# Kernel optimization log

Hardware: AMD Instinct MI355X
Metric: run time of the kernel (lower is better)

The kernel has to match this reference:

```python
import jax, jax.numpy as jnp
import numpy as np

B, S, D_IN, D = 4, 4096, 512, 256


def setup_inputs() -> dict:
    key = jax.random.key(0)
    ks = jax.random.split(key, 7)
    return {
        "query": jax.random.normal(ks[0], (B, S, D_IN), dtype=jnp.float32),
        "key": jax.random.normal(ks[1], (B, S, D_IN), dtype=jnp.float32),
        "value": jax.random.normal(ks[2], (B, S, D), dtype=jnp.float32),
        "Wq": jax.random.normal(ks[3], (D, D_IN), dtype=jnp.float32) * (1.0 / np.sqrt(D_IN)),
        "bq": jax.random.normal(ks[4], (D,), dtype=jnp.float32) * 0.01,
        "Wk": jax.random.normal(ks[5], (D, D_IN), dtype=jnp.float32) * (1.0 / np.sqrt(D_IN)),
        "bk": jax.random.normal(ks[6], (D,), dtype=jnp.float32) * 0.01,
        "scale_factor": jnp.ones((), dtype=jnp.float32),  # source uses scale_factor = 1
        "dropout_p": 0,  # fixed to 0 -> dropout is identity (deterministic baseline)
    }


def reference(query, key, value, Wq, bq, Wk, bk, scale_factor, dropout_p):
    # q/k linear projections: [B,S,512] -> [B,S,256]
    q = jnp.einsum("bsi,di->bsd", query, Wq) + bq
    k = jnp.einsum("bsi,di->bsd", key, Wk) + bk
    # scaled dot-product attention scores [B,S,S]
    scores = jnp.einsum("bqd,bkd->bqk", q, k) * scale_factor
    attn = jax.nn.softmax(scores, axis=-1)
    # dropout_p == 0 -> identity
    out = jnp.einsum("bqk,bkd->bqd", attn, value)
    return out
```

## Files before the change

### kernel.cpp

```cpp
#include <hip/hip_runtime.h>

#define S_LEN 4096
#define NROWS 16384

typedef float f32x4 __attribute__((ext_vector_type(4)));
typedef _Float16 f16x8 __attribute__((ext_vector_type(8)));

__device__ __forceinline__ unsigned short f2h(float f) {
  _Float16 h = (_Float16)f;
  return __builtin_bit_cast(unsigned short, h);
}

__device__ __forceinline__ void gload16(const void* g, void* l) {
  __builtin_amdgcn_global_load_lds(
      (const __attribute__((address_space(1))) void*)g,
      (__attribute__((address_space(3))) void*)l, 16, 0, 0);
}

__global__ void cw_kernel(const float* __restrict__ Wq, const float* __restrict__ Wk,
                          unsigned short* __restrict__ Wqb, unsigned short* __restrict__ Wkb) {
  const int i = (blockIdx.x * 256 + threadIdx.x) * 8;
  if (i >= 131072) return;
  unsigned short tmp[8] __attribute__((aligned(16)));
#pragma unroll
  for (int u = 0; u < 8; ++u) tmp[u] = f2h(Wq[i + u]);
  *(uint4*)(Wqb + i) = ((const uint4*)tmp)[0];
#pragma unroll
  for (int u = 0; u < 8; ++u) tmp[u] = f2h(Wk[i + u]);
  *(uint4*)(Wkb + i) = ((const uint4*)tmp)[0];
}

__global__ __launch_bounds__(256) void vt_kernel(const float* __restrict__ V,
                                                 unsigned short* __restrict__ Vt) {
  __shared__ float tile[64][65];
  const int tid = threadIdx.x;
  const int b = blockIdx.z, s0 = blockIdx.x * 64, d0 = blockIdx.y * 64;
  {
    const int r = tid >> 2, cs = (tid & 3) * 16;
    const float* src = V + ((long)b * S_LEN + s0 + r) * 256 + d0 + cs;
#pragma unroll
    for (int u = 0; u < 4; ++u) {
      const f32x4 v = __builtin_nontemporal_load((const f32x4*)(src + 4 * u));
      tile[r][cs + 4 * u + 0] = v[0]; tile[r][cs + 4 * u + 1] = v[1];
      tile[r][cs + 4 * u + 2] = v[2]; tile[r][cs + 4 * u + 3] = v[3];
    }
  }
  __syncthreads();
  {
    const int d = tid >> 2, ss = (tid & 3) * 16;
    unsigned short tmp[16] __attribute__((aligned(16)));
#pragma unroll
    for (int u = 0; u < 16; ++u) tmp[u] = f2h(tile[ss + u][d]);
    unsigned short* dst = Vt + ((long)b * 256 + d0 + d) * S_LEN + s0 + ss;
    *(uint4*)dst = ((const uint4*)tmp)[0];
    *((uint4*)dst + 1) = ((const uint4*)tmp)[1];
  }
}

__global__ __launch_bounds__(256, 4) void proj_kernel(
    const float* __restrict__ Xq, const float* __restrict__ Xk,
    const unsigned short* __restrict__ Wqb, const unsigned short* __restrict__ Wkb,
    const float* __restrict__ bq, const float* __restrict__ bk,
    unsigned short* __restrict__ Qb, unsigned short* __restrict__ Kb,
    const float* __restrict__ scale_ptr) {
  const int tid = threadIdx.x;
  const int lane = tid & 63, w = tid >> 6;
  const int h = lane >> 4, cc = lane & 15;
  const int z = blockIdx.y;
  const float* X = z ? Xk : Xq;
  const unsigned short* Wb = z ? Wkb : Wqb;
  const float* bias = z ? bk : bq;
  unsigned short* out = z ? Kb : Qb;
  const float sc = z ? 1.f : scale_ptr[0];
  const int rowbase = blockIdx.x * 64;

  __shared__ char sx[8192];
  __shared__ char sw[32768];

  f32x4 acc[16];
  const f32x4 fz = {0.f, 0.f, 0.f, 0.f};
#pragma unroll
  for (int nf = 0; nf < 16; ++nf) acc[nf] = fz;

  for (int kstep = 0; kstep < 8; ++kstep) {
    const int k0 = kstep * 64;
    __syncthreads();
    {
      const int r = tid >> 2;
      const int cb0 = (tid & 3) * 2;
      const float* src = X + (long)(rowbase + r) * 512 + k0 + (tid & 3) * 16;
      float xv[16];
#pragma unroll
      for (int u = 0; u < 4; ++u) {
        const f32x4 v = __builtin_nontemporal_load((const f32x4*)(src + 4 * u));
        xv[4 * u + 0] = v[0]; xv[4 * u + 1] = v[1];
        xv[4 * u + 2] = v[2]; xv[4 * u + 3] = v[3];
      }
      unsigned short tmp[16] __attribute__((aligned(16)));
#pragma unroll
      for (int u = 0; u < 16; ++u) tmp[u] = f2h(xv[u]);
      *(uint4*)(sx + r * 128 + ((cb0 ^ (r & 7)) * 16)) = ((const uint4*)tmp)[0];
      *(uint4*)(sx + r * 128 + (((cb0 + 1) ^ (r & 7)) * 16)) = ((const uint4*)tmp)[1];
    }
#pragma unroll
    for (int i = 0; i < 8; ++i) {
      const int off = w * 8192 + i * 1024 + lane * 16;
      const int row = off >> 7;
      const int lcb = (lane & 7) ^ (row & 7);
      gload16(Wb + (long)row * 512 + k0 + lcb * 8, sw + w * 8192 + i * 1024);
    }
    __syncthreads();
#pragma unroll
    for (int ks = 0; ks < 2; ++ks) {
      const int rl = 16 * w + cc;
      const f16x8 af = *(const f16x8*)(sx + rl * 128 + (((h + 4 * ks) ^ (rl & 7)) * 16));
#pragma unroll
      for (int nf = 0; nf < 16; ++nf) {
        const int n = cc + 16 * nf;
        const f16x8 bf = *(const f16x8*)(sw + n * 128 + (((h + 4 * ks) ^ (n & 7)) * 16));
        acc[nf] = __builtin_amdgcn_mfma_f32_16x16x32_f16(af, bf, acc[nf], 0, 0, 0);
      }
    }
  }
#pragma unroll
  for (int nf = 0; nf < 16; ++nf) {
    const float bv = bias[cc + 16 * nf];
#pragma unroll
    for (int r = 0; r < 4; ++r) {
      const long grow = rowbase + 16 * w + 4 * h + r;
      out[grow * 256 + cc + 16 * nf] = f2h((acc[nf][r] + bv) * sc);
    }
  }
}

__global__ __launch_bounds__(256, 2) void attn_kernel(
    const unsigned short* __restrict__ Qb, const unsigned short* __restrict__ Kb,
    const unsigned short* __restrict__ Vt, float* __restrict__ out0,
    float* __restrict__ partials, float2* __restrict__ stats,
    int* __restrict__ cnt, int nsplit, int nchunks) {
  extern __shared__ char smem[];
  const int tid = threadIdx.x;
  const int lane = tid & 63, w = tid >> 6;
  const int h = lane >> 4, c = lane & 15;

  int* s_item_p = (int*)(smem + 69632);
  if (tid == 0) {
    const unsigned x = __builtin_amdgcn_s_getreg(6164) & 7u;
    const int pref = (int)x * nchunks / 8;
    int item = 0;
    for (int k = 0; k < nchunks; ++k) {
      const int ch = (pref + k) % nchunks;
      const int t = atomicAdd(cnt + ch, 1);
      if (t < 32) { item = ch * 32 + t; break; }
    }
    *s_item_p = item;
  }
  __syncthreads();
  const int nid = *s_item_p;
  const int gqt = nid & 255;
  const int split = nid >> 8;

  const int b = gqt >> 6;
  const int qrow0 = (gqt & 63) * 64;
  const long brow = (long)b * S_LEN;

  const int kv_len = S_LEN / nsplit;
  const int kv0 = split * kv_len;
  const int nit = kv_len / 32;

  f16x8 qf[8];
  {
    const unsigned short* qbase = Qb + (brow + qrow0 + w * 16 + c) * 256 + h * 8;
#pragma unroll
    for (int kk = 0; kk < 8; ++kk)
      qf[kk] = *(const f16x8*)(qbase + kk * 32);
  }

  f32x4 O[16];
  float mrun[4], lrun[4];
  const f32x4 fz = {0.f, 0.f, 0.f, 0.f};
#pragma unroll
  for (int nfd = 0; nfd < 16; ++nfd) O[nfd] = fz;
#pragma unroll
  for (int r = 0; r < 4; ++r) { mrun[r] = -1e30f; lrun[r] = 0.f; }

  const unsigned short* kbB = Kb + brow * 256;
  const unsigned short* vbB = Vt + (long)b * 256 * S_LEN;

  auto stage = [&](int buf, int it) {
    const int kvb = kv0 + it * 32;
#pragma unroll
    for (int i = 0; i < 4; ++i) {
      const int off = i * 4096 + tid * 16;
      {
        const int row = off >> 9;
        const int lcb = ((off >> 4) & 31) ^ (row & 7);
        gload16(kbB + (long)(kvb + row) * 256 + lcb * 8, smem + buf * 16384 + off);
      }
      {
        const int drow = off >> 6;
        const int lcb = ((off >> 4) & 3) ^ ((drow >> 1) & 3);
        gload16(vbB + (long)drow * S_LEN + kvb + lcb * 8,
                smem + 32768 + buf * 16384 + off);
      }
    }
  };

  char* const pt = smem + 65536 + w * 1024;

  stage(0, 0);
  __syncthreads();

  for (int t = 0; t < nit; ++t) {
    const int buf = t & 1;
    if (t + 1 < nit) stage(buf ^ 1, t + 1);
    const char* kt = smem + buf * 16384;
    const char* vl = smem + 32768 + buf * 16384;

    f32x4 s[2];
    s[0] = fz; s[1] = fz;
    __builtin_amdgcn_s_setprio(1);
#pragma unroll
    for (int kk = 0; kk < 8; ++kk) {
#pragma unroll
      for (int nf = 0; nf < 2; ++nf) {
        const int r = c + 16 * nf;
        const int cb = ((4 * kk + h) ^ (r & 7)) & 31;
        const f16x8 kf = *(const f16x8*)(kt + r * 512 + cb * 16);
        s[nf] = __builtin_amdgcn_mfma_f32_16x16x32_f16(qf[kk], kf, s[nf], 0, 0, 0);
      }
    }
    __builtin_amdgcn_s_setprio(0);

    {
      bool ok = true;
#pragma unroll
      for (int r = 0; r < 4; ++r)
        ok &= (fmaxf(s[0][r], s[1][r]) <= mrun[r] + 8.f);
      if (__all(ok)) {
#pragma unroll
        for (int r = 0; r < 4; ++r) {
          const float p0 = __expf(s[0][r] - mrun[r]);
          const float p1 = __expf(s[1][r] - mrun[r]);
          s[0][r] = p0; s[1][r] = p1;
          lrun[r] += p0 + p1;
        }
      } else {
#pragma unroll
        for (int r = 0; r < 4; ++r) {
          float mx = fmaxf(s[0][r], s[1][r]);
          mx = fmaxf(mx, __shfl_xor(mx, 1));
          mx = fmaxf(mx, __shfl_xor(mx, 2));
          mx = fmaxf(mx, __shfl_xor(mx, 4));
          mx = fmaxf(mx, __shfl_xor(mx, 8));
          const float mnew = fmaxf(mrun[r], mx);
          const float alpha = __expf(mrun[r] - mnew);
          const float p0 = __expf(s[0][r] - mnew);
          const float p1 = __expf(s[1][r] - mnew);
          s[0][r] = p0; s[1][r] = p1;
          lrun[r] = lrun[r] * alpha + p0 + p1;
          mrun[r] = mnew;
#pragma unroll
          for (int nfd = 0; nfd < 16; ++nfd) O[nfd][r] *= alpha;
        }
      }
#pragma unroll
      for (int nf = 0; nf < 2; ++nf)
#pragma unroll
        for (int r = 0; r < 4; ++r) {
          const int C = c + 16 * nf;
          const int blk = ((C >> 3) ^ r ^ h) & 3;
          *(unsigned short*)(pt + (4 * h + r) * 64 + blk * 16 + (C & 7) * 2) =
              f2h(s[nf][r]);
        }
    }
    asm volatile("" ::: "memory");

    __builtin_amdgcn_s_setprio(1);
    {
      const f16x8 pa = *(const f16x8*)(pt + c * 64 + (((h ^ c ^ (c >> 2)) & 3) * 16));
#pragma unroll
      for (int nfd = 0; nfd < 16; ++nfd) {
        const int dr = c + 16 * nfd;
        const f16x8 vf = *(const f16x8*)(vl + dr * 64 + (((h ^ (dr >> 1)) & 3) * 16));
        O[nfd] = __builtin_amdgcn_mfma_f32_16x16x32_f16(pa, vf, O[nfd], 0, 0, 0);
      }
    }
    __builtin_amdgcn_s_setprio(0);
    __syncthreads();
  }

#pragma unroll
  for (int r = 0; r < 4; ++r) {
    float l = lrun[r];
    l += __shfl_xor(l, 1); l += __shfl_xor(l, 2);
    l += __shfl_xor(l, 4); l += __shfl_xor(l, 8);
    lrun[r] = l;
  }

  const long rowg0 = brow + qrow0 + w * 16 + 4 * h;
  if (nsplit == 1) {
    float inv[4];
#pragma unroll
    for (int r = 0; r < 4; ++r) inv[r] = 1.f / lrun[r];
#pragma unroll
    for (int nfd = 0; nfd < 16; ++nfd)
#pragma unroll
      for (int r = 0; r < 4; ++r)
        out0[(rowg0 + r) * 256 + c + 16 * nfd] = O[nfd][r] * inv[r];
  } else {
    float* dst = (split == 0) ? out0 : (partials + (long)(split - 1) * NROWS * 256);
#pragma unroll
    for (int nfd = 0; nfd < 16; ++nfd)
#pragma unroll
      for (int r = 0; r < 4; ++r)
        dst[(rowg0 + r) * 256 + c + 16 * nfd] = O[nfd][r];
    if (c == 0) {
#pragma unroll
      for (int r = 0; r < 4; ++r)
        stats[(long)split * NROWS + rowg0 + r] = make_float2(mrun[r], lrun[r]);
    }
  }
}

__global__ __launch_bounds__(256) void merge_kernel(float* __restrict__ out0,
                                                    const float* __restrict__ partials,
                                                    const float2* __restrict__ stats,
                                                    int nsplit) {
  const int i4 = blockIdx.x * 256 + threadIdx.x;
  const int row = i4 >> 6;
  float2 st[4];
#pragma unroll
  for (int s = 0; s < 4; ++s)
    st[s] = (s < nsplit) ? stats[s * NROWS + row] : make_float2(-1e30f, 0.f);
  const float m = fmaxf(fmaxf(st[0].x, st[1].x), fmaxf(st[2].x, st[3].x));
  float e[4], den = 0.f;
#pragma unroll
  for (int s = 0; s < 4; ++s) { e[s] = __expf(st[s].x - m); den += st[s].y * e[s]; }
  const float invd = 1.f / den;
  float ax = 0.f, ay = 0.f, az = 0.f, aw = 0.f;
#pragma unroll
  for (int s = 0; s < 4; ++s) {
    if (s < nsplit) {
      const float* src = (s == 0) ? (const float*)out0
                                  : partials + (long)(s - 1) * NROWS * 256;
      const f32x4 v = ((const f32x4*)src)[i4];
      ax += v[0] * e[s]; ay += v[1] * e[s]; az += v[2] * e[s]; aw += v[3] * e[s];
    }
  }
  const f32x4 res = {ax * invd, ay * invd, az * invd, aw * invd};
  ((f32x4*)out0)[i4] = res;
}

extern "C" void kernel_launch(void* const* d_in, const int* in_sizes, int n_in,
                              void* d_out, int out_size, void* d_ws, size_t ws_size,
                              hipStream_t stream) {
  const float* query = (const float*)d_in[0];
  const float* key   = (const float*)d_in[1];
  const float* value = (const float*)d_in[2];
  const float* Wq    = (const float*)d_in[3];
  const float* bq    = (const float*)d_in[4];
  const float* Wk    = (const float*)d_in[5];
  const float* bk    = (const float*)d_in[6];
  const float* scale = (const float*)d_in[7];
  float* out = (float*)d_out;

  char* ws = (char*)d_ws;
  unsigned short* Wqb = (unsigned short*)(ws);
  unsigned short* Wkb = (unsigned short*)(ws + 262144);
  unsigned short* Qb  = (unsigned short*)(ws + 524288);
  unsigned short* Kb  = (unsigned short*)(ws + 8912896);
  unsigned short* Vt  = (unsigned short*)(ws + 17301504);
  int* cnt            = (int*)(ws + 25690112);
  float2* stats       = (float2*)(ws + 25694208);
  float* partials     = (float*)(ws + 26218496);

  int nsplit = 1;
  if (ws_size >= 42995712) nsplit = 2;
  const int nblk = 256 * nsplit;
  const int nchunks = nblk / 32;

  hipMemsetAsync(cnt, 0, 64, stream);
  cw_kernel<<<64, 256, 0, stream>>>(Wq, Wk, Wqb, Wkb);
  vt_kernel<<<dim3(64, 4, 4), 256, 0, stream>>>(value, Vt);
  proj_kernel<<<dim3(256, 2), 256, 0, stream>>>(query, key, Wqb, Wkb, bq, bk, Qb, Kb, scale);

  hipFuncSetAttribute((const void*)attn_kernel,
                      hipFuncAttributeMaxDynamicSharedMemorySize, 69648);
  attn_kernel<<<nblk, 256, 69648, stream>>>(Qb, Kb, Vt, out, partials,
                                            stats, cnt, nsplit, nchunks);
  if (nsplit > 1)
    merge_kernel<<<4096, 256, 0, stream>>>(out, partials, stats, nsplit);
}
```

Before: 186.3 us.

## Split attention warps into 2x2 query/KV tiles with shared softmax and exp2

The attention kernel now arranges its four waves as pairs. Each pair handles 32 query rows, and within a pair each wave takes half of the 32-key tile and half of the output D columns. K fragments are loaded once and reused across two query m-tiles, and V fragments are reused the same way, which cuts LDS reads per MFMA. The cost is extra block barriers each iteration: one for a block-wide fast-path vote, one for exchanging row maxima, and one for the shared P tile. The query scale is also premultiplied by log2(e) so exp2f can replace __expf, and merge is updated to match.

```diff
diff --git a/kernel.cpp b/kernel.cpp
--- a/kernel.cpp
+++ b/kernel.cpp
@@ -71,7 +71,7 @@
   const unsigned short* Wb = z ? Wkb : Wqb;
   const float* bias = z ? bk : bq;
   unsigned short* out = z ? Kb : Qb;
-  const float sc = z ? 1.f : scale_ptr[0];
+  const float sc = z ? 1.f : scale_ptr[0] * 1.44269504088896340736f;
   const int rowbase = blockIdx.x * 64;
 
   __shared__ char sx[8192];
@@ -142,8 +142,9 @@
   const int tid = threadIdx.x;
   const int lane = tid & 63, w = tid >> 6;
   const int h = lane >> 4, c = lane & 15;
-
-  int* s_item_p = (int*)(smem + 69632);
+  const int p = w >> 1, kvh = w & 1;
+
+  int* s_item_p = (int*)(smem + 71184);
   if (tid == 0) {
     const unsigned x = __builtin_amdgcn_s_getreg(6164) & 7u;
     const int pref = (int)x * nchunks / 8;
@@ -168,21 +169,26 @@
   const int kv0 = split * kv_len;
   const int nit = kv_len / 32;
 
-  f16x8 qf[8];
+  f16x8 qf[2][8];
   {
-    const unsigned short* qbase = Qb + (brow + qrow0 + w * 16 + c) * 256 + h * 8;
-#pragma unroll
-    for (int kk = 0; kk < 8; ++kk)
-      qf[kk] = *(const f16x8*)(qbase + kk * 32);
-  }
-
-  f32x4 O[16];
-  float mrun[4], lrun[4];
+    const unsigned short* qbase = Qb + (brow + qrow0 + p * 32 + c) * 256 + h * 8;
+#pragma unroll
+    for (int m = 0; m < 2; ++m)
+#pragma unroll
+      for (int kk = 0; kk < 8; ++kk)
+        qf[m][kk] = *(const f16x8*)(qbase + m * 4096 + kk * 32);
+  }
+
+  f32x4 O[2][8];
+  float mrun[2][4], lrun[2][4];
   const f32x4 fz = {0.f, 0.f, 0.f, 0.f};
 #pragma unroll
-  for (int nfd = 0; nfd < 16; ++nfd) O[nfd] = fz;
-#pragma unroll
-  for (int r = 0; r < 4; ++r) { mrun[r] = -1e30f; lrun[r] = 0.f; }
+  for (int m = 0; m < 2; ++m) {
+#pragma unroll
+    for (int nfd = 0; nfd < 8; ++nfd) O[m][nfd] = fz;
+#pragma unroll
+    for (int r = 0; r < 4; ++r) { mrun[m][r] = -1e30f; lrun[m][r] = 0.f; }
+  }
 
   const unsigned short* kbB = Kb + brow * 256;
   const unsigned short* vbB = Vt + (long)b * 256 * S_LEN;
@@ -206,7 +212,9 @@
     }
   };
 
-  char* const pt = smem + 65536 + w * 1024;
+  char* const ppt = smem + 65536 + p * 2560;
+  float* const comm = (float*)(smem + 70656 + p * 256);
+  int* const okb = (int*)(smem + 71168);
 
   stage(0, 0);
   __syncthreads();
@@ -222,68 +230,91 @@
     __builtin_amdgcn_s_setprio(1);
 #pragma unroll
     for (int kk = 0; kk < 8; ++kk) {
-#pragma unroll
-      for (int nf = 0; nf < 2; ++nf) {
-        const int r = c + 16 * nf;
-        const int cb = ((4 * kk + h) ^ (r & 7)) & 31;
-        const f16x8 kf = *(const f16x8*)(kt + r * 512 + cb * 16);
-        s[nf] = __builtin_amdgcn_mfma_f32_16x16x32_f16(qf[kk], kf, s[nf], 0, 0, 0);
-      }
+      const int krow = kvh * 16 + c;
+      const int cb = ((4 * kk + h) ^ (c & 7)) & 31;
+      const f16x8 kf = *(const f16x8*)(kt + krow * 512 + cb * 16);
+      s[0] = __builtin_amdgcn_mfma_f32_16x16x32_f16(qf[0][kk], kf, s[0], 0, 0, 0);
+      s[1] = __builtin_amdgcn_mfma_f32_16x16x32_f16(qf[1][kk], kf, s[1], 0, 0, 0);
     }
     __builtin_amdgcn_s_setprio(0);
 
-    {
-      bool ok = true;
-#pragma unroll
-      for (int r = 0; r < 4; ++r)
-        ok &= (fmaxf(s[0][r], s[1][r]) <= mrun[r] + 8.f);
-      if (__all(ok)) {
+    bool ok = true;
+#pragma unroll
+    for (int m = 0; m < 2; ++m)
+#pragma unroll
+      for (int r = 0; r < 4; ++r) ok &= (s[m][r] <= mrun[m][r] + 8.f);
+    const int okw = __all(ok) ? 1 : 0;
+    if (lane == 0) okb[w] = okw;
+    asm volatile("s_waitcnt lgkmcnt(0)" ::: "memory");
+    __builtin_amdgcn_sched_barrier(0);
+    __builtin_amdgcn_s_barrier();
+    const int blockfast = okb[0] & okb[1] & okb[2] & okb[3];
+
+    if (blockfast) {
+#pragma unroll
+      for (int m = 0; m < 2; ++m)
 #pragma unroll
         for (int r = 0; r < 4; ++r) {
-          const float p0 = __expf(s[0][r] - mrun[r]);
-          const float p1 = __expf(s[1][r] - mrun[r]);
-          s[0][r] = p0; s[1][r] = p1;
-          lrun[r] += p0 + p1;
+          const float pp = exp2f(s[m][r] - mrun[m][r]);
+          lrun[m][r] += pp;
+          *(unsigned short*)(ppt + (16 * m + 4 * h + r) * 80 + kvh * 32 + c * 2) =
+              f2h(pp);
         }
-      } else {
+    } else {
+      float lm[2][4];
+#pragma unroll
+      for (int m = 0; m < 2; ++m)
 #pragma unroll
         for (int r = 0; r < 4; ++r) {
-          float mx = fmaxf(s[0][r], s[1][r]);
+          float mx = s[m][r];
           mx = fmaxf(mx, __shfl_xor(mx, 1));
           mx = fmaxf(mx, __shfl_xor(mx, 2));
           mx = fmaxf(mx, __shfl_xor(mx, 4));
           mx = fmaxf(mx, __shfl_xor(mx, 8));
-          const float mnew = fmaxf(mrun[r], mx);
-          const float alpha = __expf(mrun[r] - mnew);
-          const float p0 = __expf(s[0][r] - mnew);
-          const float p1 = __expf(s[1][r] - mnew);
-          s[0][r] = p0; s[1][r] = p1;
-          lrun[r] = lrun[r] * alpha + p0 + p1;
-          mrun[r] = mnew;
-#pragma unroll
-          for (int nfd = 0; nfd < 16; ++nfd) O[nfd][r] *= alpha;
+          lm[m][r] = mx;
         }
-      }
-#pragma unroll
-      for (int nf = 0; nf < 2; ++nf)
+      if (c == 0) {
+#pragma unroll
+        for (int m = 0; m < 2; ++m)
+#pragma unroll
+          for (int r = 0; r < 4; ++r)
+            comm[kvh * 32 + 16 * m + 4 * h + r] = lm[m][r];
+      }
+      asm volatile("s_waitcnt lgkmcnt(0)" ::: "memory");
+      __builtin_amdgcn_sched_barrier(0);
+      __builtin_amdgcn_s_barrier();
+#pragma unroll
+      for (int m = 0; m < 2; ++m)
 #pragma unroll
         for (int r = 0; r < 4; ++r) {
-          const int C = c + 16 * nf;
-          const int blk = ((C >> 3) ^ r ^ h) & 3;
-          *(unsigned short*)(pt + (4 * h + r) * 64 + blk * 16 + (C & 7) * 2) =
-              f2h(s[nf][r]);
+          const float pmx = comm[(kvh ^ 1) * 32 + 16 * m + 4 * h + r];
+          const float mnew = fmaxf(mrun[m][r], fmaxf(lm[m][r], pmx));
+          const float alpha = exp2f(mrun[m][r] - mnew);
+          const float pp = exp2f(s[m][r] - mnew);
+          lrun[m][r] = lrun[m][r] * alpha + pp;
+          mrun[m][r] = mnew;
+#pragma unroll
+          for (int nfd = 0; nfd < 8; ++nfd) O[m][nfd][r] *= alpha;
+          *(unsigned short*)(ppt + (16 * m + 4 * h + r) * 80 + kvh * 32 + c * 2) =
+              f2h(pp);
         }
     }
-    asm volatile("" ::: "memory");
+    asm volatile("s_waitcnt lgkmcnt(0)" ::: "memory");
+    __builtin_amdgcn_sched_barrier(0);
+    __builtin_amdgcn_s_barrier();
 
     __builtin_amdgcn_s_setprio(1);
     {
-      const f16x8 pa = *(const f16x8*)(pt + c * 64 + (((h ^ c ^ (c >> 2)) & 3) * 16));
-#pragma unroll
-      for (int nfd = 0; nfd < 16; ++nfd) {
-        const int dr = c + 16 * nfd;
+      f16x8 pa[2];
+#pragma unroll
+      for (int m = 0; m < 2; ++m)
+        pa[m] = *(const f16x8*)(ppt + (16 * m + c) * 80 + h * 16);
+#pragma unroll
+      for (int nfd = 0; nfd < 8; ++nfd) {
+        const int dr = kvh * 128 + c + 16 * nfd;
         const f16x8 vf = *(const f16x8*)(vl + dr * 64 + (((h ^ (dr >> 1)) & 3) * 16));
-        O[nfd] = __builtin_amdgcn_mfma_f32_16x16x32_f16(pa, vf, O[nfd], 0, 0, 0);
+        O[0][nfd] = __builtin_amdgcn_mfma_f32_16x16x32_f16(pa[0], vf, O[0][nfd], 0, 0, 0);
+        O[1][nfd] = __builtin_amdgcn_mfma_f32_16x16x32_f16(pa[1], vf, O[1][nfd], 0, 0, 0);
       }
     }
     __builtin_amdgcn_s_setprio(0);
@@ -291,34 +322,59 @@
   }
 
 #pragma unroll
-  for (int r = 0; r < 4; ++r) {
-    float l = lrun[r];
-    l += __shfl_xor(l, 1); l += __shfl_xor(l, 2);
-    l += __shfl_xor(l, 4); l += __shfl_xor(l, 8);
-    lrun[r] = l;
-  }
-
-  const long rowg0 = brow + qrow0 + w * 16 + 4 * h;
+  for (int m = 0; m < 2; ++m)
+#pragma unroll
+    for (int r = 0; r < 4; ++r) {
+      float l = lrun[m][r];
+      l += __shfl_xor(l, 1); l += __shfl_xor(l, 2);
+      l += __shfl_xor(l, 4); l += __shfl_xor(l, 8);
+      lrun[m][r] = l;
+    }
+  if (c == 0) {
+#pragma unroll
+    for (int m = 0; m < 2; ++m)
+#pragma unroll
+      for (int r = 0; r < 4; ++r)
+        comm[kvh * 32 + 16 * m + 4 * h + r] = lrun[m][r];
+  }
+  __syncthreads();
+  float lt[2][4];
+#pragma unroll
+  for (int m = 0; m < 2; ++m)
+#pragma unroll
+    for (int r = 0; r < 4; ++r)
+      lt[m][r] = lrun[m][r] + comm[(kvh ^ 1) * 32 + 16 * m + 4 * h + r];
+
+  const long rowg0 = brow + qrow0 + p * 32 + 4 * h;
   if (nsplit == 1) {
-    float inv[4];
-#pragma unroll
-    for (int r = 0; r < 4; ++r) inv[r] = 1.f / lrun[r];
-#pragma unroll
-    for (int nfd = 0; nfd < 16; ++nfd)
-#pragma unroll
-      for (int r = 0; r < 4; ++r)
-        out0[(rowg0 + r) * 256 + c + 16 * nfd] = O[nfd][r] * inv[r];
+#pragma unroll
+    for (int m = 0; m < 2; ++m) {
+      float inv[4];
+#pragma unroll
+      for (int r = 0; r < 4; ++r) inv[r] = 1.f / lt[m][r];
+#pragma unroll
+      for (int nfd = 0; nfd < 8; ++nfd)
+#pragma unroll
+        for (int r = 0; r < 4; ++r)
+          out0[(rowg0 + 16 * m + r) * 256 + kvh * 128 + c + 16 * nfd] =
+              O[m][nfd][r] * inv[r];
+    }
   } else {
     float* dst = (split == 0) ? out0 : (partials + (long)(split - 1) * NROWS * 256);
 #pragma unroll
-    for (int nfd = 0; nfd < 16; ++nfd)
-#pragma unroll
-      for (int r = 0; r < 4; ++r)
-        dst[(rowg0 + r) * 256 + c + 16 * nfd] = O[nfd][r];
-    if (c == 0) {
-#pragma unroll
-      for (int r = 0; r < 4; ++r)
-        stats[(long)split * NROWS + rowg0 + r] = make_float2(mrun[r], lrun[r]);
+    for (int m = 0; m < 2; ++m)
+#pragma unroll
+      for (int nfd = 0; nfd < 8; ++nfd)
+#pragma unroll
+        for (int r = 0; r < 4; ++r)
+          dst[(rowg0 + 16 * m + r) * 256 + kvh * 128 + c + 16 * nfd] = O[m][nfd][r];
+    if (kvh == 0 && c == 0) {
+#pragma unroll
+      for (int m = 0; m < 2; ++m)
+#pragma unroll
+        for (int r = 0; r < 4; ++r)
+          stats[(long)split * NROWS + rowg0 + 16 * m + r] =
+              make_float2(mrun[m][r], lt[m][r]);
     }
   }
 }
@@ -336,7 +392,7 @@
   const float m = fmaxf(fmaxf(st[0].x, st[1].x), fmaxf(st[2].x, st[3].x));
   float e[4], den = 0.f;
 #pragma unroll
-  for (int s = 0; s < 4; ++s) { e[s] = __expf(st[s].x - m); den += st[s].y * e[s]; }
+  for (int s = 0; s < 4; ++s) { e[s] = exp2f(st[s].x - m); den += st[s].y * e[s]; }
   const float invd = 1.f / den;
   float ax = 0.f, ay = 0.f, az = 0.f, aw = 0.f;
 #pragma unroll
@@ -386,8 +442,8 @@
   proj_kernel<<<dim3(256, 2), 256, 0, stream>>>(query, key, Wqb, Wkb, bq, bk, Qb, Kb, scale);
 
   hipFuncSetAttribute((const void*)attn_kernel,
-                      hipFuncAttributeMaxDynamicSharedMemorySize, 69648);
-  attn_kernel<<<nblk, 256, 69648, stream>>>(Qb, Kb, Vt, out, partials,
+                      hipFuncAttributeMaxDynamicSharedMemorySize, 71200);
+  attn_kernel<<<nblk, 256, 71200, stream>>>(Qb, Kb, Vt, out, partials,
                                             stats, cnt, nsplit, nchunks);
   if (nsplit > 1)
     merge_kernel<<<4096, 256, 0, stream>>>(out, partials, stats, nsplit);
```

Result: slower. 226.3 us (+21.5%).

## Split attention head dim across blocks, use exp2 softmax, raise occupancy and kv splits

Applied to the files above, without the earlier changes.

Each attention block now computes only half of the 256-wide output dimension, so the O accumulator and the V shared-memory staging are halved. This lets three blocks fit per CU and doubles the block count, and up to four KV splits are allowed when the workspace is large enough. The 1/ln2 factor is folded into the Q projection so the softmax uses exp2f directly. In exchange, QK^T scores are computed twice per query tile (once per half) and K is loaded twice, while the merge handles more partials.

```diff
diff --git a/kernel.cpp b/kernel.cpp
--- a/kernel.cpp
+++ b/kernel.cpp
@@ -71,7 +71,7 @@
   const unsigned short* Wb = z ? Wkb : Wqb;
   const float* bias = z ? bk : bq;
   unsigned short* out = z ? Kb : Qb;
-  const float sc = z ? 1.f : scale_ptr[0];
+  const float sc = z ? 1.f : scale_ptr[0] * 1.44269504088896340736f;
   const int rowbase = blockIdx.x * 64;
 
   __shared__ char sx[8192];
@@ -133,7 +133,7 @@
   }
 }
 
-__global__ __launch_bounds__(256, 2) void attn_kernel(
+__global__ __launch_bounds__(256, 3) void attn_kernel(
     const unsigned short* __restrict__ Qb, const unsigned short* __restrict__ Kb,
     const unsigned short* __restrict__ Vt, float* __restrict__ out0,
     float* __restrict__ partials, float2* __restrict__ stats,
@@ -143,7 +143,7 @@
   const int lane = tid & 63, w = tid >> 6;
   const int h = lane >> 4, c = lane & 15;
 
-  int* s_item_p = (int*)(smem + 69632);
+  int* s_item_p = (int*)(smem + 53248);
   if (tid == 0) {
     const unsigned x = __builtin_amdgcn_s_getreg(6164) & 7u;
     const int pref = (int)x * nchunks / 8;
@@ -157,11 +157,12 @@
   }
   __syncthreads();
   const int nid = *s_item_p;
-  const int gqt = nid & 255;
-  const int split = nid >> 8;
-
-  const int b = gqt >> 6;
-  const int qrow0 = (gqt & 63) * 64;
+  const int split = nid >> 9;
+  const int qt = (nid & 511) >> 1;
+  const int dh = nid & 1;
+
+  const int b = qt >> 6;
+  const int qrow0 = (qt & 63) * 64;
   const long brow = (long)b * S_LEN;
 
   const int kv_len = S_LEN / nsplit;
@@ -176,16 +177,16 @@
       qf[kk] = *(const f16x8*)(qbase + kk * 32);
   }
 
-  f32x4 O[16];
+  f32x4 O[8];
   float mrun[4], lrun[4];
   const f32x4 fz = {0.f, 0.f, 0.f, 0.f};
 #pragma unroll
-  for (int nfd = 0; nfd < 16; ++nfd) O[nfd] = fz;
+  for (int nfd = 0; nfd < 8; ++nfd) O[nfd] = fz;
 #pragma unroll
   for (int r = 0; r < 4; ++r) { mrun[r] = -1e30f; lrun[r] = 0.f; }
 
   const unsigned short* kbB = Kb + brow * 256;
-  const unsigned short* vbB = Vt + (long)b * 256 * S_LEN;
+  const unsigned short* vbB = Vt + ((long)b * 256 + dh * 128) * S_LEN;
 
   auto stage = [&](int buf, int it) {
     const int kvb = kv0 + it * 32;
@@ -197,16 +198,16 @@
         const int lcb = ((off >> 4) & 31) ^ (row & 7);
         gload16(kbB + (long)(kvb + row) * 256 + lcb * 8, smem + buf * 16384 + off);
       }
-      {
+      if (i < 2) {
         const int drow = off >> 6;
         const int lcb = ((off >> 4) & 3) ^ ((drow >> 1) & 3);
         gload16(vbB + (long)drow * S_LEN + kvb + lcb * 8,
-                smem + 32768 + buf * 16384 + off);
+                smem + 32768 + buf * 8192 + off);
       }
     }
   };
 
-  char* const pt = smem + 65536 + w * 1024;
+  char* const pt = smem + 49152 + w * 1024;
 
   stage(0, 0);
   __syncthreads();
@@ -215,7 +216,7 @@
     const int buf = t & 1;
     if (t + 1 < nit) stage(buf ^ 1, t + 1);
     const char* kt = smem + buf * 16384;
-    const char* vl = smem + 32768 + buf * 16384;
+    const char* vl = smem + 32768 + buf * 8192;
 
     f32x4 s[2];
     s[0] = fz; s[1] = fz;
@@ -240,8 +241,8 @@
       if (__all(ok)) {
 #pragma unroll
         for (int r = 0; r < 4; ++r) {
-          const float p0 = __expf(s[0][r] - mrun[r]);
-          const float p1 = __expf(s[1][r] - mrun[r]);
+          const float p0 = exp2f(s[0][r] - mrun[r]);
+          const float p1 = exp2f(s[1][r] - mrun[r]);
           s[0][r] = p0; s[1][r] = p1;
           lrun[r] += p0 + p1;
         }
@@ -254,14 +255,14 @@
           mx = fmaxf(mx, __shfl_xor(mx, 4));
           mx = fmaxf(mx, __shfl_xor(mx, 8));
           const float mnew = fmaxf(mrun[r], mx);
-          const float alpha = __expf(mrun[r] - mnew);
-          const float p0 = __expf(s[0][r] - mnew);
-          const float p1 = __expf(s[1][r] - mnew);
+          const float alpha = exp2f(mrun[r] - mnew);
+          const float p0 = exp2f(s[0][r] - mnew);
+          const float p1 = exp2f(s[1][r] - mnew);
           s[0][r] = p0; s[1][r] = p1;
           lrun[r] = lrun[r] * alpha + p0 + p1;
           mrun[r] = mnew;
 #pragma unroll
-          for (int nfd = 0; nfd < 16; ++nfd) O[nfd][r] *= alpha;
+          for (int nfd = 0; nfd < 8; ++nfd) O[nfd][r] *= alpha;
         }
       }
 #pragma unroll
@@ -280,7 +281,7 @@
     {
       const f16x8 pa = *(const f16x8*)(pt + c * 64 + (((h ^ c ^ (c >> 2)) & 3) * 16));
 #pragma unroll
-      for (int nfd = 0; nfd < 16; ++nfd) {
+      for (int nfd = 0; nfd < 8; ++nfd) {
         const int dr = c + 16 * nfd;
         const f16x8 vf = *(const f16x8*)(vl + dr * 64 + (((h ^ (dr >> 1)) & 3) * 16));
         O[nfd] = __builtin_amdgcn_mfma_f32_16x16x32_f16(pa, vf, O[nfd], 0, 0, 0);
@@ -299,23 +300,24 @@
   }
 
   const long rowg0 = brow + qrow0 + w * 16 + 4 * h;
+  const int colbase = dh * 128 + c;
   if (nsplit == 1) {
     float inv[4];
 #pragma unroll
     for (int r = 0; r < 4; ++r) inv[r] = 1.f / lrun[r];
 #pragma unroll
-    for (int nfd = 0; nfd < 16; ++nfd)
+    for (int nfd = 0; nfd < 8; ++nfd)
 #pragma unroll
       for (int r = 0; r < 4; ++r)
-        out0[(rowg0 + r) * 256 + c + 16 * nfd] = O[nfd][r] * inv[r];
+        out0[(rowg0 + r) * 256 + colbase + 16 * nfd] = O[nfd][r] * inv[r];
   } else {
     float* dst = (split == 0) ? out0 : (partials + (long)(split - 1) * NROWS * 256);
 #pragma unroll
-    for (int nfd = 0; nfd < 16; ++nfd)
+    for (int nfd = 0; nfd < 8; ++nfd)
 #pragma unroll
       for (int r = 0; r < 4; ++r)
-        dst[(rowg0 + r) * 256 + c + 16 * nfd] = O[nfd][r];
-    if (c == 0) {
+        dst[(rowg0 + r) * 256 + colbase + 16 * nfd] = O[nfd][r];
+    if (dh == 0 && c == 0) {
 #pragma unroll
       for (int r = 0; r < 4; ++r)
         stats[(long)split * NROWS + rowg0 + r] = make_float2(mrun[r], lrun[r]);
@@ -336,7 +338,7 @@
   const float m = fmaxf(fmaxf(st[0].x, st[1].x), fmaxf(st[2].x, st[3].x));
   float e[4], den = 0.f;
 #pragma unroll
-  for (int s = 0; s < 4; ++s) { e[s] = __expf(st[s].x - m); den += st[s].y * e[s]; }
+  for (int s = 0; s < 4; ++s) { e[s] = exp2f(st[s].x - m); den += st[s].y * e[s]; }
   const float invd = 1.f / den;
   float ax = 0.f, ay = 0.f, az = 0.f, aw = 0.f;
 #pragma unroll
@@ -376,18 +378,19 @@
   float* partials     = (float*)(ws + 26218496);
 
   int nsplit = 1;
-  if (ws_size >= 42995712) nsplit = 2;
-  const int nblk = 256 * nsplit;
+  if (ws_size >= 76550144) nsplit = 4;
+  else if (ws_size >= 42995712) nsplit = 2;
+  const int nblk = 512 * nsplit;
   const int nchunks = nblk / 32;
 
-  hipMemsetAsync(cnt, 0, 64, stream);
+  hipMemsetAsync(cnt, 0, 256, stream);
   cw_kernel<<<64, 256, 0, stream>>>(Wq, Wk, Wqb, Wkb);
   vt_kernel<<<dim3(64, 4, 4), 256, 0, stream>>>(value, Vt);
   proj_kernel<<<dim3(256, 2), 256, 0, stream>>>(query, key, Wqb, Wkb, bq, bk, Qb, Kb, scale);
 
   hipFuncSetAttribute((const void*)attn_kernel,
-                      hipFuncAttributeMaxDynamicSharedMemorySize, 69648);
-  attn_kernel<<<nblk, 256, 69648, stream>>>(Qb, Kb, Vt, out, partials,
+                      hipFuncAttributeMaxDynamicSharedMemorySize, 53264);
+  attn_kernel<<<nblk, 256, 53264, stream>>>(Qb, Kb, Vt, out, partials,
                                             stats, cnt, nsplit, nchunks);
   if (nsplit > 1)
     merge_kernel<<<4096, 256, 0, stream>>>(out, partials, stats, nsplit);
```

Result: slower. 300.4 us (+61.3%).
